# Kernel optimization log

Hardware: AMD Instinct MI355X
Metric: run time of the kernel (lower is better)

Reference implementation:

```python
import jax, jax.numpy as jnp
import numpy as np

B, T, D, H, L, V = 64, 512, 1024, 512, 2, 32000
RESET = 32  # hidden state zeroed every 32 steps (ei > 0 and ei % 32 == 0)


def setup_inputs() -> dict:
    key = jax.random.key(0)
    ks = jax.random.split(key, 10)
    s = 1.0 / np.sqrt(H)
    u = lambda k, shp: jax.random.uniform(k, shp, jnp.float32, -s, s)
    return {
        'rt': jax.random.randint(ks[0], (B, T), 0, V),
        're': jax.random.randint(ks[1], (B, T), 0, V),
        'rm': jax.random.randint(ks[2], (B, T), 0, V),
        'h0': jnp.zeros((L, 2, B, H), jnp.float32),
        'c0': jnp.zeros((L, 2, B, H), jnp.float32),
        'E_rt': jax.random.normal(ks[3], (V, D), jnp.float32) * 0.02,
        'E_re': jax.random.normal(ks[4], (V, D), jnp.float32) * 0.02,
        'E_rm': jax.random.normal(ks[5], (V, D), jnp.float32) * 0.02,
        'Wih': u(ks[6], (L, 2, 4 * H, D)),
        'Whh': u(ks[7], (L, 2, 4 * H, H)),
        'bih': u(ks[8], (L, 2, 4 * H)),
        'bhh': u(ks[9], (L, 2, 4 * H)),
    }


def _lstm_scan(x_seq, h0, c0, Wih, Whh, bih, bhh):
    # x_seq: [T, B, D]; h0/c0: [L, 2, B, H]
    bias = (bih + bhh)[:, :, None, :]  # [L, 2, 1, 4H]

    def step(carry, inp):
        h, c = carry
        x, t = inp
        reset = jnp.logical_and(t > 0, t % RESET == 0)
        h = jnp.where(reset, 0.0, h)
        c = jnp.where(reset, 0.0, c)
        new_h, new_c = [], []
        layer_in = x  # [B, D]
        for l in range(L):
            # both directions step forward in time (faithful to per-step bilstm call)
            g = (jnp.einsum('bd,xgd->xbg', layer_in, Wih[l])
                 + jnp.einsum('xbh,xgh->xbg', h[l], Whh[l])
                 + bias[l])  # [2, B, 4H]
            i, f, gg, o = jnp.split(g, 4, axis=-1)  # PyTorch gate order i,f,g,o
            cc = jax.nn.sigmoid(f) * c[l] + jax.nn.sigmoid(i) * jnp.tanh(gg)
            hh = jax.nn.sigmoid(o) * jnp.tanh(cc)
            new_h.append(hh)
            new_c.append(cc)
            layer_in = jnp.concatenate([hh[0], hh[1]], axis=-1)  # [B, 2H] = [B, D]
        return (jnp.stack(new_h), jnp.stack(new_c)), layer_in

    (hT, cT), out = jax.lax.scan(step, (h0, c0), (x_seq, jnp.arange(x_seq.shape[0])))
    return out, hT, cT  # out: [T, B, D]


def reference(rt, re, rm, h0, c0, E_rt, E_re, E_rm, Wih, Whh, bih, bhh):
    emb = E_rt[rt] + E_re[re] + E_rm[rm]  # [B, T, D]
    out, hT, cT = _lstm_scan(jnp.transpose(emb, (1, 0, 2)), h0, c0, Wih, Whh, bih, bhh)
    outputs = jnp.transpose(out, (1, 0, 2))  # [B, T, D]
    hidden = (hT.reshape(L * 2, B, H), cT.reshape(L * 2, B, H))
    return outputs, hidden
```

## Files before the change

### kernel.cpp

```cpp
#include <hip/hip_runtime.h>
#include <hip/hip_bf16.h>
#include <stdint.h>


typedef _Float16 half8 __attribute__((ext_vector_type(8)));
typedef _Float16 half4v __attribute__((ext_vector_type(4)));
typedef float float4v __attribute__((ext_vector_type(4)));

#define AS1C(p) ((const __attribute__((address_space(1))) void*)(p))
#define AS3(p)  ((__attribute__((address_space(3))) void*)(p))

__device__ __forceinline__ float sigm(float x){ return 1.0f/(1.0f + __expf(-x)); }
__device__ __forceinline__ float tanh_f(float x){ return 2.0f/(1.0f + __expf(-2.0f*x)) - 1.0f; }

__global__ __launch_bounds__(256) void k_embed(
    const int* __restrict__ rt, const int* __restrict__ re, const int* __restrict__ rm,
    const float* __restrict__ Ert, const float* __restrict__ Ere, const float* __restrict__ Erm,
    _Float16* __restrict__ emb)
{
  size_t idx = (size_t)blockIdx.x * 256 + threadIdx.x;
  int dq = (int)(idx & 255);
  size_t bt = idx >> 8;
  size_t bt2 = bt + 16384;
  int a0 = rt[bt],  a1 = re[bt],  a2 = rm[bt];
  int b0 = rt[bt2], b1 = re[bt2], b2 = rm[bt2];
  float4 u0 = ((const float4*)Ert)[(size_t)a0 * 256 + dq];
  float4 u1 = ((const float4*)Ere)[(size_t)a1 * 256 + dq];
  float4 u2 = ((const float4*)Erm)[(size_t)a2 * 256 + dq];
  float4 w0 = ((const float4*)Ert)[(size_t)b0 * 256 + dq];
  float4 w1 = ((const float4*)Ere)[(size_t)b1 * 256 + dq];
  float4 w2 = ((const float4*)Erm)[(size_t)b2 * 256 + dq];
  half4v h, g;
  h[0] = (_Float16)(u0.x + u1.x + u2.x);
  h[1] = (_Float16)(u0.y + u1.y + u2.y);
  h[2] = (_Float16)(u0.z + u1.z + u2.z);
  h[3] = (_Float16)(u0.w + u1.w + u2.w);
  g[0] = (_Float16)(w0.x + w1.x + w2.x);
  g[1] = (_Float16)(w0.y + w1.y + w2.y);
  g[2] = (_Float16)(w0.z + w1.z + w2.z);
  g[3] = (_Float16)(w0.w + w1.w + w2.w);
  int b_ = (int)(bt >> 9), t_ = (int)(bt & 511);
  ((half4v*)emb)[((size_t)t_ * 64 + b_) * 256 + dq] = h;
  ((half4v*)emb)[((size_t)t_ * 64 + (b_ + 32)) * 256 + dq] = g;
}

__global__ __launch_bounds__(256) void k_prepw(
    const float* __restrict__ Wih, const float* __restrict__ Whh,
    _Float16* __restrict__ Wc)
{
  int bid = blockIdx.x;
  int ld = bid >> 11;
  int n  = bid & 2047;
  int g  = (n >> 4) & 3;
  int j  = ((n >> 6) << 4) | (n & 15);
  int srow = g * 512 + j;
  const float* sx = Wih + ((size_t)ld * 2048 + srow) * 1024;
  const float* sh = Whh + ((size_t)ld * 2048 + srow) * 512;
  _Float16* dst = Wc + ((size_t)ld * 2048 + n) * 1536;
  for (int k = threadIdx.x; k < 1536; k += 256)
    dst[k] = (_Float16)(k < 1024 ? sx[k] : sh[k - 1024]);
}

__global__ __launch_bounds__(256) void k_prepb(
    const float* __restrict__ bih, const float* __restrict__ bhh,
    float* __restrict__ biasc)
{
  int idx = blockIdx.x * 256 + threadIdx.x;
  int ld = idx >> 11, n = idx & 2047;
  int g = (n >> 4) & 3;
  int j = ((n >> 6) << 4) | (n & 15);
  int srow = ld * 2048 + g * 512 + j;
  biasc[idx] = bih[srow] + bhh[srow];
}

__global__ __launch_bounds__(256) void k_init(
    int layer, const float* __restrict__ h0, const float* __restrict__ c0,
    _Float16* __restrict__ hbuf, float* __restrict__ cbuf)
{
  int idx = blockIdx.x * 256 + threadIdx.x;
  int dir = idx >> 19;
  int rj = idx & ((1 << 19) - 1);
  int r = rj >> 9, j = rj & 511;
  float hv = 0.f, cv = 0.f;
  if (r < 64) {
    size_t s0 = ((size_t)(layer * 2 + dir) * 64 + r) * 512 + j;
    hv = h0[s0]; cv = c0[s0];
  }
  hbuf[idx] = (_Float16)hv;
  cbuf[idx] = cv;
}

__global__ __launch_bounds__(512, 4) void k_step(
    int s0, int s1,
    const _Float16* __restrict__ emb,
    _Float16* __restrict__ out0,
    float* __restrict__ outs,
    _Float16* __restrict__ hbAll,
    float* __restrict__ cbAll,
    const _Float16* __restrict__ Wc,
    const float* __restrict__ biasc,
    float* __restrict__ hT, float* __restrict__ cT)
{
  const int layer = blockIdx.z;
  const int s = layer ? s1 : s0;
  if ((unsigned)s > 31u) return;
  const _Float16* xsrc = layer ? out0 : emb;
  const _Float16* hin  = hbAll + ((size_t)(layer * 2 + (s & 1))) * 1048576;
  _Float16*       hout = hbAll + ((size_t)(layer * 2 + ((s & 1) ^ 1))) * 1048576;
  float*          cbuf = cbAll + (size_t)layer * 1048576;

  __shared__ __align__(16) _Float16 smem[32768];
  const int tid = threadIdx.x;
  const int w = tid >> 6, l = tid & 63;
  const int nb = blockIdx.x;
  const int m0 = blockIdx.y * 128;
  const int dir = nb >> 4;
  const int n0 = (nb & 15) * 128;
  const int ld = layer * 2 + dir;

  const char* pX[4]; const char* pH[4]; uint32_t ldsoff[4];
  #pragma unroll
  for (int ii = 0; ii < 4; ++ii) {
    int instr = w * 4 + ii;
    if (instr < 16) {
      int c = instr * 64 + l;
      int row = c & 127, kc = c >> 7;
      int r = m0 + row;
      int erow = ((r >> 6) * 32 + s) * 64 + (r & 63);
      pX[ii] = (const char*)(xsrc + (size_t)erow * 1024 + kc * 8);
      pH[ii] = (const char*)(hin + ((size_t)dir * 1024 + r) * 512 + kc * 8) - 2048;
      ldsoff[ii] = (uint32_t)instr * 1024u;
    } else {
      int c = (instr - 16) * 64 + l;
      int nl = c & 127, kc = c >> 7;
      const char* p = (const char*)(Wc + ((size_t)ld * 2048 + n0 + nl) * 1536 + kc * 8);
      pX[ii] = p; pH[ii] = p;
      ldsoff[ii] = 16384u + (uint32_t)(instr - 16) * 1024u;
    }
  }

  const int wm = w >> 1, wn = w & 1;
  float4v acc[2][4];
  const float4v vzero = {0.f, 0.f, 0.f, 0.f};
  #pragma unroll
  for (int mf = 0; mf < 2; ++mf)
    #pragma unroll
    for (int nf = 0; nf < 4; ++nf) acc[mf][nf] = vzero;

  auto stage = [&](int it, int buf) {
    const int k0 = it * 64;
    const bool isx = (it < 16);
    #pragma unroll
    for (int ii = 0; ii < 4; ++ii) {
      const char* src = (isx ? pX[ii] : pH[ii]) + (size_t)k0 * 2;
      __builtin_amdgcn_global_load_lds(AS1C(src),
          AS3(((char*)smem) + (size_t)buf * 32768 + ldsoff[ii]), 16, 0, 0);
    }
  };

  stage(0, 0);
  #pragma unroll 2
  for (int it = 0; it < 24; ++it) {
    const int cur = it & 1;
    if (it < 23) {
      stage(it + 1, cur ^ 1);
      asm volatile("s_waitcnt vmcnt(4)" ::: "memory");
    } else {
      asm volatile("s_waitcnt vmcnt(0)" ::: "memory");
    }
    __builtin_amdgcn_sched_barrier(0);
    __builtin_amdgcn_s_barrier();
    __builtin_amdgcn_sched_barrier(0);

    const _Float16* sA = smem + (size_t)cur * 16384;
    const _Float16* sB = sA + 8192;
    __builtin_amdgcn_s_setprio(1);
    #pragma unroll
    for (int kk = 0; kk < 64; kk += 32) {
      const int kcb = (kk >> 3) + (l >> 4);
      half8 a[2], b[4];
      #pragma unroll
      for (int mf = 0; mf < 2; ++mf)
        a[mf] = *(const half8*)(sA + ((size_t)kcb * 128 + wm * 32 + mf * 16 + (l & 15)) * 8);
      #pragma unroll
      for (int nf = 0; nf < 4; ++nf)
        b[nf] = *(const half8*)(sB + ((size_t)kcb * 128 + wn * 64 + nf * 16 + (l & 15)) * 8);
      #pragma unroll
      for (int mf = 0; mf < 2; ++mf)
        #pragma unroll
        for (int nf = 0; nf < 4; ++nf)
          acc[mf][nf] = __builtin_amdgcn_mfma_f32_16x16x32_f16(a[mf], b[nf], acc[mf][nf], 0, 0, 0);
    }
    __builtin_amdgcn_s_setprio(0);
    asm volatile("s_waitcnt lgkmcnt(0)" ::: "memory");
    __builtin_amdgcn_sched_barrier(0);
    __builtin_amdgcn_s_barrier();
    __builtin_amdgcn_sched_barrier(0);
  }

  const int q = (nb & 15) * 2 + wn;
  const int jj = l & 15;
  const int j = q * 16 + jj;
  const int bb_base = ld * 2048 + n0 + wn * 64;
  const float bias_i = biasc[bb_base + 0 * 16 + jj];
  const float bias_f = biasc[bb_base + 1 * 16 + jj];
  const float bias_g = biasc[bb_base + 2 * 16 + jj];
  const float bias_o = biasc[bb_base + 3 * 16 + jj];

  #pragma unroll
  for (int mf = 0; mf < 2; ++mf) {
    #pragma unroll
    for (int reg = 0; reg < 4; ++reg) {
      int r = m0 + wm * 32 + mf * 16 + (l >> 4) * 4 + reg;
      float ip = acc[mf][0][reg] + bias_i;
      float fp = acc[mf][1][reg] + bias_f;
      float gp = acc[mf][2][reg] + bias_g;
      float op = acc[mf][3][reg] + bias_o;
      size_t cidx = ((size_t)dir * 1024 + r) * 512 + j;
      float cold = cbuf[cidx];
      float cn = sigm(fp) * cold + sigm(ip) * tanh_f(gp);
      float hn = sigm(op) * tanh_f(cn);
      cbuf[cidx] = cn;
      hout[cidx] = (_Float16)hn;
      int chunk = r >> 6, bb = r & 63;
      int t = chunk * 32 + s;
      if (layer == 0) {
        out0[((size_t)t * 64 + bb) * 1024 + dir * 512 + j] = (_Float16)hn;
      } else {
        outs[((size_t)bb * 512 + t) * 1024 + dir * 512 + j] = hn;
      }
      if (s == 31 && chunk == 15) {
        size_t hidx = ((size_t)(layer * 2 + dir) * 64 + bb) * 512 + j;
        hT[hidx] = hn; cT[hidx] = cn;
      }
    }
  }
}

extern "C" void kernel_launch(void* const* d_in, const int* in_sizes, int n_in,
                              void* d_out, int out_size, void* d_ws, size_t ws_size,
                              hipStream_t stream)
{
  const int*   rt  = (const int*)d_in[0];
  const int*   re  = (const int*)d_in[1];
  const int*   rm  = (const int*)d_in[2];
  const float* h0  = (const float*)d_in[3];
  const float* c0  = (const float*)d_in[4];
  const float* Ert = (const float*)d_in[5];
  const float* Ere = (const float*)d_in[6];
  const float* Erm = (const float*)d_in[7];
  const float* Wih = (const float*)d_in[8];
  const float* Whh = (const float*)d_in[9];
  const float* bih = (const float*)d_in[10];
  const float* bhh = (const float*)d_in[11];

  float* outs = (float*)d_out;
  float* hT = outs + (size_t)64 * 512 * 1024;
  float* cT = hT + (size_t)4 * 64 * 512;

  char* p = (char*)d_ws;
  _Float16* emb  = (_Float16*)p;  p += (size_t)32768 * 1024 * 2;
  _Float16* out0 = (_Float16*)p;  p += (size_t)32768 * 1024 * 2;
  _Float16* Wc   = (_Float16*)p;  p += (size_t)4 * 2048 * 1536 * 2;
  float*    biasc= (float*)p;     p += (size_t)4 * 2048 * 4;
  _Float16* hbAll= (_Float16*)p;  p += (size_t)4 * 1048576 * 2;
  float*    cbAll= (float*)p;     p += (size_t)2 * 1048576 * 4;

  k_prepw<<<8192, 256, 0, stream>>>(Wih, Whh, Wc);
  k_prepb<<<32, 256, 0, stream>>>(bih, bhh, biasc);
  k_embed<<<16384, 256, 0, stream>>>(rt, re, rm, Ert, Ere, Erm, emb);
  k_init<<<4096, 256, 0, stream>>>(0, h0, c0, hbAll, cbAll);
  k_init<<<4096, 256, 0, stream>>>(1, h0, c0, hbAll + (size_t)2 * 1048576,
                                   cbAll + (size_t)1048576);

  for (int k = 0; k < 33; ++k) {
    k_step<<<dim3(32, 8, 2), 512, 0, stream>>>(k, k - 1, emb, out0, outs,
                                               hbAll, cbAll, Wc, biasc, hT, cT);
  }
}
```

Baseline: 2.254 ms.

## Hoist input projection out of recurrent step into batched 4-step GEMMs

Splits the combined weight into separate input (Wx) and recurrent (Wh) matrices and adds a k_xp kernel that computes x·Wih+bias for four timesteps at a time into an fp16 ring buffer. The recurrent step kernel now only does the H=512 recurrent GEMM (8 k-iterations instead of 24) and adds the precomputed projection in the epilogue. Layer 1 lags layer 0 by four steps so its inputs can be batched, and layer-0 outputs go through an 8-slot ring. The aim is to shorten the serial critical path. The cost is extra launches, storing the projection and bias sum in fp16, and tight ring-slot reuse ordering.

```diff
diff --git a/kernel.cpp b/kernel.cpp
--- a/kernel.cpp
+++ b/kernel.cpp
@@ -46,19 +46,19 @@
 
 __global__ __launch_bounds__(256) void k_prepw(
     const float* __restrict__ Wih, const float* __restrict__ Whh,
-    _Float16* __restrict__ Wc)
+    _Float16* __restrict__ Wx, _Float16* __restrict__ Wh)
 {
   int bid = blockIdx.x;
-  int ld = bid >> 11;
-  int n  = bid & 2047;
-  int g  = (n >> 4) & 3;
-  int j  = ((n >> 6) << 4) | (n & 15);
+  int ld = bid >> 11, n = bid & 2047;
+  int g = (n >> 4) & 3;
+  int j = ((n >> 6) << 4) | (n & 15);
   int srow = g * 512 + j;
   const float* sx = Wih + ((size_t)ld * 2048 + srow) * 1024;
   const float* sh = Whh + ((size_t)ld * 2048 + srow) * 512;
-  _Float16* dst = Wc + ((size_t)ld * 2048 + n) * 1536;
-  for (int k = threadIdx.x; k < 1536; k += 256)
-    dst[k] = (_Float16)(k < 1024 ? sx[k] : sh[k - 1024]);
+  _Float16* dx = Wx + (size_t)bid * 1024;
+  _Float16* dh = Wh + (size_t)bid * 512;
+  for (int k = threadIdx.x; k < 1024; k += 256) dx[k] = (_Float16)sx[k];
+  for (int k = threadIdx.x; k < 512;  k += 256) dh[k] = (_Float16)sh[k];
 }
 
 __global__ __launch_bounds__(256) void k_prepb(
@@ -90,21 +90,137 @@
   cbuf[idx] = cv;
 }
 
+__global__ __launch_bounds__(512, 4) void k_xp(
+    int layer, int batch,
+    const _Float16* __restrict__ emb, const _Float16* __restrict__ out0ring,
+    const _Float16* __restrict__ Wx, const float* __restrict__ biasc,
+    _Float16* __restrict__ xpring)
+{
+  __shared__ __align__(16) _Float16 smem[32768];
+  const int tid = threadIdx.x;
+  const int w = tid >> 6, l = tid & 63;
+  const int n0 = blockIdx.x * 128;
+  const int by = blockIdx.y;
+  const int sIdx = by >> 3;
+  const int rbase = (by & 7) * 128;
+  const int s = batch * 4 + sIdx;
+  const int slot = s % 12;
+
+  const char* pG[4]; uint32_t ldsoff[4];
+  #pragma unroll
+  for (int ii = 0; ii < 4; ++ii) {
+    int instr = w * 4 + ii;
+    if (instr < 16) {
+      int c = instr * 64 + l;
+      int row = c & 127, kc = c >> 7;
+      int r = rbase + row;
+      if (layer == 0) {
+        int t = (r >> 6) * 32 + s;
+        pG[ii] = (const char*)(emb + ((size_t)t * 64 + (r & 63)) * 1024 + kc * 8);
+      } else {
+        pG[ii] = (const char*)(out0ring + ((size_t)(s & 7) * 1024 + r) * 1024 + kc * 8);
+      }
+      ldsoff[ii] = (uint32_t)instr * 1024u;
+    } else {
+      int c = (instr - 16) * 64 + l;
+      int nl = c & 127, kc = c >> 7;
+      int ng = n0 + nl;
+      int ldb = layer * 2 + (ng >> 11);
+      pG[ii] = (const char*)(Wx + ((size_t)ldb * 2048 + (ng & 2047)) * 1024 + kc * 8);
+      ldsoff[ii] = 16384u + (uint32_t)(instr - 16) * 1024u;
+    }
+  }
+
+  const int wm = w >> 1, wn = w & 1;
+  float4v acc[2][4];
+  const float4v vzero = {0.f, 0.f, 0.f, 0.f};
+  #pragma unroll
+  for (int mf = 0; mf < 2; ++mf)
+    #pragma unroll
+    for (int nf = 0; nf < 4; ++nf) acc[mf][nf] = vzero;
+
+  auto stage = [&](int it, int buf) {
+    #pragma unroll
+    for (int ii = 0; ii < 4; ++ii)
+      __builtin_amdgcn_global_load_lds(AS1C(pG[ii] + (size_t)it * 128),
+          AS3(((char*)smem) + (size_t)buf * 32768 + ldsoff[ii]), 16, 0, 0);
+  };
+
+  stage(0, 0);
+  #pragma unroll 2
+  for (int it = 0; it < 16; ++it) {
+    const int cur = it & 1;
+    if (it < 15) {
+      stage(it + 1, cur ^ 1);
+      asm volatile("s_waitcnt vmcnt(4)" ::: "memory");
+    } else {
+      asm volatile("s_waitcnt vmcnt(0)" ::: "memory");
+    }
+    __builtin_amdgcn_sched_barrier(0);
+    __builtin_amdgcn_s_barrier();
+    __builtin_amdgcn_sched_barrier(0);
+    const _Float16* sA = smem + (size_t)cur * 16384;
+    const _Float16* sB = sA + 8192;
+    __builtin_amdgcn_s_setprio(1);
+    #pragma unroll
+    for (int kk = 0; kk < 64; kk += 32) {
+      const int kcb = (kk >> 3) + (l >> 4);
+      half8 a[2], b[4];
+      #pragma unroll
+      for (int mf = 0; mf < 2; ++mf)
+        a[mf] = *(const half8*)(sA + ((size_t)kcb * 128 + wm * 32 + mf * 16 + (l & 15)) * 8);
+      #pragma unroll
+      for (int nf = 0; nf < 4; ++nf)
+        b[nf] = *(const half8*)(sB + ((size_t)kcb * 128 + wn * 64 + nf * 16 + (l & 15)) * 8);
+      #pragma unroll
+      for (int mf = 0; mf < 2; ++mf)
+        #pragma unroll
+        for (int nf = 0; nf < 4; ++nf)
+          acc[mf][nf] = __builtin_amdgcn_mfma_f32_16x16x32_f16(a[mf], b[nf], acc[mf][nf], 0, 0, 0);
+    }
+    __builtin_amdgcn_s_setprio(0);
+    asm volatile("s_waitcnt lgkmcnt(0)" ::: "memory");
+    __builtin_amdgcn_sched_barrier(0);
+    __builtin_amdgcn_s_barrier();
+    __builtin_amdgcn_sched_barrier(0);
+  }
+
+  const int jj = l & 15;
+  const int ldb = layer * 2 + (n0 >> 11);
+  float bias[4];
+  #pragma unroll
+  for (int nf = 0; nf < 4; ++nf)
+    bias[nf] = biasc[ldb * 2048 + ((n0 & 2047) + wn * 64 + nf * 16 + jj)];
+  #pragma unroll
+  for (int mf = 0; mf < 2; ++mf)
+    #pragma unroll
+    for (int reg = 0; reg < 4; ++reg) {
+      int row = rbase + wm * 32 + mf * 16 + (l >> 4) * 4 + reg;
+      #pragma unroll
+      for (int nf = 0; nf < 4; ++nf) {
+        int n4 = n0 + wn * 64 + nf * 16 + jj;
+        xpring[((size_t)slot * 1024 + row) * 4096 + n4] =
+            (_Float16)(acc[mf][nf][reg] + bias[nf]);
+      }
+    }
+}
+
 __global__ __launch_bounds__(512, 4) void k_step(
     int s0, int s1,
-    const _Float16* __restrict__ emb,
-    _Float16* __restrict__ out0,
+    _Float16* __restrict__ out0ring,
     float* __restrict__ outs,
     _Float16* __restrict__ hbAll,
     float* __restrict__ cbAll,
-    const _Float16* __restrict__ Wc,
-    const float* __restrict__ biasc,
+    const _Float16* __restrict__ Wh,
+    const _Float16* __restrict__ xp0ring,
+    const _Float16* __restrict__ xp1ring,
     float* __restrict__ hT, float* __restrict__ cT)
 {
   const int layer = blockIdx.z;
   const int s = layer ? s1 : s0;
   if ((unsigned)s > 31u) return;
-  const _Float16* xsrc = layer ? out0 : emb;
+
+  const _Float16* xp   = (layer ? xp1ring : xp0ring) + (size_t)(s % 12) * 1024 * 4096;
   const _Float16* hin  = hbAll + ((size_t)(layer * 2 + (s & 1))) * 1048576;
   _Float16*       hout = hbAll + ((size_t)(layer * 2 + ((s & 1) ^ 1))) * 1048576;
   float*          cbuf = cbAll + (size_t)layer * 1048576;
@@ -118,7 +234,7 @@
   const int n0 = (nb & 15) * 128;
   const int ld = layer * 2 + dir;
 
-  const char* pX[4]; const char* pH[4]; uint32_t ldsoff[4];
+  const char* pG[4]; uint32_t ldsoff[4];
   #pragma unroll
   for (int ii = 0; ii < 4; ++ii) {
     int instr = w * 4 + ii;
@@ -126,15 +242,12 @@
       int c = instr * 64 + l;
       int row = c & 127, kc = c >> 7;
       int r = m0 + row;
-      int erow = ((r >> 6) * 32 + s) * 64 + (r & 63);
-      pX[ii] = (const char*)(xsrc + (size_t)erow * 1024 + kc * 8);
-      pH[ii] = (const char*)(hin + ((size_t)dir * 1024 + r) * 512 + kc * 8) - 2048;
+      pG[ii] = (const char*)(hin + ((size_t)dir * 1024 + r) * 512 + kc * 8);
       ldsoff[ii] = (uint32_t)instr * 1024u;
     } else {
       int c = (instr - 16) * 64 + l;
       int nl = c & 127, kc = c >> 7;
-      const char* p = (const char*)(Wc + ((size_t)ld * 2048 + n0 + nl) * 1536 + kc * 8);
-      pX[ii] = p; pH[ii] = p;
+      pG[ii] = (const char*)(Wh + ((size_t)ld * 2048 + n0 + nl) * 512 + kc * 8);
       ldsoff[ii] = 16384u + (uint32_t)(instr - 16) * 1024u;
     }
   }
@@ -148,21 +261,17 @@
     for (int nf = 0; nf < 4; ++nf) acc[mf][nf] = vzero;
 
   auto stage = [&](int it, int buf) {
-    const int k0 = it * 64;
-    const bool isx = (it < 16);
-    #pragma unroll
-    for (int ii = 0; ii < 4; ++ii) {
-      const char* src = (isx ? pX[ii] : pH[ii]) + (size_t)k0 * 2;
-      __builtin_amdgcn_global_load_lds(AS1C(src),
+    #pragma unroll
+    for (int ii = 0; ii < 4; ++ii)
+      __builtin_amdgcn_global_load_lds(AS1C(pG[ii] + (size_t)it * 128),
           AS3(((char*)smem) + (size_t)buf * 32768 + ldsoff[ii]), 16, 0, 0);
-    }
   };
 
   stage(0, 0);
-  #pragma unroll 2
-  for (int it = 0; it < 24; ++it) {
+  #pragma unroll
+  for (int it = 0; it < 8; ++it) {
     const int cur = it & 1;
-    if (it < 23) {
+    if (it < 7) {
       stage(it + 1, cur ^ 1);
       asm volatile("s_waitcnt vmcnt(4)" ::: "memory");
     } else {
@@ -171,7 +280,6 @@
     __builtin_amdgcn_sched_barrier(0);
     __builtin_amdgcn_s_barrier();
     __builtin_amdgcn_sched_barrier(0);
-
     const _Float16* sA = smem + (size_t)cur * 16384;
     const _Float16* sB = sA + 8192;
     __builtin_amdgcn_s_setprio(1);
@@ -201,21 +309,18 @@
   const int q = (nb & 15) * 2 + wn;
   const int jj = l & 15;
   const int j = q * 16 + jj;
-  const int bb_base = ld * 2048 + n0 + wn * 64;
-  const float bias_i = biasc[bb_base + 0 * 16 + jj];
-  const float bias_f = biasc[bb_base + 1 * 16 + jj];
-  const float bias_g = biasc[bb_base + 2 * 16 + jj];
-  const float bias_o = biasc[bb_base + 3 * 16 + jj];
+  const int n4b = dir * 2048 + n0 + wn * 64 + jj;
 
   #pragma unroll
   for (int mf = 0; mf < 2; ++mf) {
     #pragma unroll
     for (int reg = 0; reg < 4; ++reg) {
       int r = m0 + wm * 32 + mf * 16 + (l >> 4) * 4 + reg;
-      float ip = acc[mf][0][reg] + bias_i;
-      float fp = acc[mf][1][reg] + bias_f;
-      float gp = acc[mf][2][reg] + bias_g;
-      float op = acc[mf][3][reg] + bias_o;
+      const _Float16* xr = xp + (size_t)r * 4096 + n4b;
+      float ip = acc[mf][0][reg] + (float)xr[0];
+      float fp = acc[mf][1][reg] + (float)xr[16];
+      float gp = acc[mf][2][reg] + (float)xr[32];
+      float op = acc[mf][3][reg] + (float)xr[48];
       size_t cidx = ((size_t)dir * 1024 + r) * 512 + j;
       float cold = cbuf[cidx];
       float cn = sigm(fp) * cold + sigm(ip) * tanh_f(gp);
@@ -225,7 +330,7 @@
       int chunk = r >> 6, bb = r & 63;
       int t = chunk * 32 + s;
       if (layer == 0) {
-        out0[((size_t)t * 64 + bb) * 1024 + dir * 512 + j] = (_Float16)hn;
+        out0ring[((size_t)(s & 7) * 1024 + r) * 1024 + dir * 512 + j] = (_Float16)hn;
       } else {
         outs[((size_t)bb * 512 + t) * 1024 + dir * 512 + j] = hn;
       }
@@ -259,22 +364,34 @@
   float* cT = hT + (size_t)4 * 64 * 512;
 
   char* p = (char*)d_ws;
-  _Float16* emb  = (_Float16*)p;  p += (size_t)32768 * 1024 * 2;
-  _Float16* out0 = (_Float16*)p;  p += (size_t)32768 * 1024 * 2;
-  _Float16* Wc   = (_Float16*)p;  p += (size_t)4 * 2048 * 1536 * 2;
-  float*    biasc= (float*)p;     p += (size_t)4 * 2048 * 4;
-  _Float16* hbAll= (_Float16*)p;  p += (size_t)4 * 1048576 * 2;
-  float*    cbAll= (float*)p;     p += (size_t)2 * 1048576 * 4;
-
-  k_prepw<<<8192, 256, 0, stream>>>(Wih, Whh, Wc);
+  _Float16* emb   = (_Float16*)p; p += (size_t)32768 * 1024 * 2;
+  _Float16* Wx    = (_Float16*)p; p += (size_t)4 * 2048 * 1024 * 2;
+  _Float16* Wh    = (_Float16*)p; p += (size_t)4 * 2048 * 512 * 2;
+  float*    biasc = (float*)p;    p += (size_t)4 * 2048 * 4;
+  _Float16* out0r = (_Float16*)p; p += (size_t)8 * 1024 * 1024 * 2;
+  _Float16* hbAll = (_Float16*)p; p += (size_t)4 * 1048576 * 2;
+  float*    cbAll = (float*)p;    p += (size_t)2 * 1048576 * 4;
+  _Float16* xp0r  = (_Float16*)p; p += (size_t)12 * 1024 * 4096 * 2;
+  _Float16* xp1r  = (_Float16*)p; p += (size_t)12 * 1024 * 4096 * 2;
+
+  k_prepw<<<8192, 256, 0, stream>>>(Wih, Whh, Wx, Wh);
   k_prepb<<<32, 256, 0, stream>>>(bih, bhh, biasc);
   k_embed<<<16384, 256, 0, stream>>>(rt, re, rm, Ert, Ere, Erm, emb);
   k_init<<<4096, 256, 0, stream>>>(0, h0, c0, hbAll, cbAll);
   k_init<<<4096, 256, 0, stream>>>(1, h0, c0, hbAll + (size_t)2 * 1048576,
                                    cbAll + (size_t)1048576);
 
-  for (int k = 0; k < 33; ++k) {
-    k_step<<<dim3(32, 8, 2), 512, 0, stream>>>(k, k - 1, emb, out0, outs,
-                                               hbAll, cbAll, Wc, biasc, hT, cT);
-  }
-}
+  k_xp<<<dim3(32, 32), 512, 0, stream>>>(0, 0, emb, out0r, Wx, biasc, xp0r);
+  k_xp<<<dim3(32, 32), 512, 0, stream>>>(0, 1, emb, out0r, Wx, biasc, xp0r);
+
+  for (int k = 0; k < 36; ++k) {
+    if (k > 0 && (k & 3) == 0) {
+      int b = k / 4 + 1;
+      if (b < 8) k_xp<<<dim3(32, 32), 512, 0, stream>>>(0, b, emb, out0r, Wx, biasc, xp0r);
+    }
+    k_step<<<dim3(32, 8, 2), 512, 0, stream>>>(k, k - 4, out0r, outs,
+                                               hbAll, cbAll, Wh, xp0r, xp1r, hT, cT);
+    if ((k & 3) == 3 && k < 32)
+      k_xp<<<dim3(32, 32), 512, 0, stream>>>(1, (k - 3) / 4, emb, out0r, Wx, biasc, xp1r);
+  }
+}
```

After: 2.485 ms. 1.1x slower.
